# Optimization experiments

Hardware: AMD Instinct MI355X
Metric: run time of the kernel (lower is better)

The kernel has to match this reference:

```python
import jax, jax.numpy as jnp
import numpy as np

M = 16          # num_particles
EPS = 0.006


def setup_inputs() -> dict:
    key = jax.random.key(0)
    k1, k2, k3, k4 = jax.random.split(key, 4)
    B, P, O = 131072, 16, 4  # batch, pred_horizon, obs_horizon
    return {
        "ys_t": jax.random.normal(k1, (B, P, O), dtype=jnp.float32),
        "ys_r_stop": jax.random.normal(k2, (B, P, O), dtype=jnp.float32),
        "w_scale": jax.random.uniform(k3, (B,), dtype=jnp.float32),
        "time_weights": jax.random.uniform(k4, (B,), dtype=jnp.float32),
    }


def _laplace(a, b, ws, D):
    # a,b: [G, M, D]; ws: [G, M] (scale indexed by j, the first particle index)
    d = jnp.linalg.norm(a[:, :, None, :] - b[:, None, :, :], axis=-1)  # [G, M, M]
    d = jnp.maximum(d, EPS)
    return jnp.exp(-ws[:, :, None] * d / D)


def reference(ys_t, ys_r_stop, w_scale, time_weights):
    B = ys_t.shape[0]
    G = B // M
    x = ys_t.reshape(G, M, -1)        # [G, M, D]
    y = ys_r_stop.reshape(G, M, -1)   # [G, M, D]
    D = x.shape[-1]                   # pred_horizon * obs_horizon (dim_normalize)
    ws = w_scale.reshape(G, M)
    tw = time_weights.reshape(G, M)[:, 0]  # [G]
    terms = _laplace(x, x, ws, D) + _laplace(y, y, ws, D) - 2.0 * _laplace(x, y, ws, D)
    group_loss = terms.sum(axis=(1, 2)) * tw / (M * M)  # [G]
    return group_loss.sum() / G
```

## Files before the change

### kernel.cpp

```cpp
#include <hip/hip_runtime.h>


#define EPS_D 0.006f

#define ROT(v, O) __int_as_float(__builtin_amdgcn_update_dpp(              \
        0, __float_as_int(v), 0x120 + (O), 0xF, 0xF, false))

__global__ __launch_bounds__(256, 4)
void imm_loss_kernel(const float* __restrict__ ys_t,
                     const float* __restrict__ ys_r,
                     const float* __restrict__ w_scale,
                     const float* __restrict__ time_w,
                     float* __restrict__ partials)
{
    const int tid  = threadIdx.x;
    const int lane = tid & 63;
    const int wave = tid >> 6;
    const int g    = blockIdx.x * 4 + wave;
    const int j    = lane & 15;
    const int db   = lane >> 4;

    __shared__ float4 lds4[4][512];

    const float4* xg = reinterpret_cast<const float4*>(ys_t + (size_t)g * 1024);
    const float4* yg = reinterpret_cast<const float4*>(ys_r + (size_t)g * 1024);

    float4 xs[4], yv[4];
    #pragma unroll
    for (int k = 0; k < 4; ++k) {
        const int r  = 4 * k + db;
        const int gq = j ^ (r & 7);
        xs[k] = xg[r * 16 + gq];
        yv[k] = yg[r * 16 + gq];
    }
    #pragma unroll
    for (int k = 0; k < 4; ++k) {
        lds4[wave][k * 64 + lane]       = xs[k];
        lds4[wave][256 + k * 64 + lane] = yv[k];
    }

    const float s_j = w_scale[g * 16 + j] * (1.0f / 64.0f);
    const float tw  = time_w[g * 16];

    float xarr[16], yarr[16];
    #pragma unroll
    for (int m = 0; m < 4; ++m) {
        const int sl = (db * 4 + m) ^ (j & 7);
        const float4 xv = lds4[wave][j * 16 + sl];
        const float4 yw = lds4[wave][256 + j * 16 + sl];
        xarr[4*m+0] = xv.x; xarr[4*m+1] = xv.y; xarr[4*m+2] = xv.z; xarr[4*m+3] = xv.w;
        yarr[4*m+0] = yw.x; yarr[4*m+1] = yw.y; yarr[4*m+2] = yw.z; yarr[4*m+3] = yw.w;
    }

    float nx = 0.f, ny = 0.f, g0 = 0.f;
    float gxx[8], gyy[8], gxy[8], hxy[7];
    #pragma unroll
    for (int i = 0; i < 8; ++i) { gxx[i] = 0.f; gyy[i] = 0.f; gxy[i] = 0.f; }
    #pragma unroll
    for (int i = 0; i < 7; ++i) hxy[i] = 0.f;

#define ACC_FULL(O) {                                                      \
            const float xr = ROT(xd, O);                                   \
            const float yr = ROT(yd, O);                                   \
            gxx[(O)-1] = fmaf(xr, xd, gxx[(O)-1]);                         \
            gyy[(O)-1] = fmaf(yr, yd, gyy[(O)-1]);                         \
            gxy[(O)-1] = fmaf(yr, xd, gxy[(O)-1]); }
#define ACC_XY(O) {                                                        \
            const float yr = ROT(yd, O);                                   \
            hxy[(O)-9] = fmaf(yr, xd, hxy[(O)-9]); }

    #pragma unroll
    for (int d = 0; d < 16; ++d) {
        const float xd = xarr[d], yd = yarr[d];
        nx = fmaf(xd, xd, nx);
        ny = fmaf(yd, yd, ny);
        g0 = fmaf(xd, yd, g0);
        ACC_FULL(1) ACC_FULL(2) ACC_FULL(3) ACC_FULL(4)
        ACC_FULL(5) ACC_FULL(6) ACC_FULL(7) ACC_FULL(8)
        ACC_XY(9)  ACC_XY(10) ACC_XY(11) ACC_XY(12)
        ACC_XY(13) ACC_XY(14) ACC_XY(15)
    }

#define RED(v) { v += __shfl_xor(v, 16, 64); v += __shfl_xor(v, 32, 64); }
    RED(nx) RED(ny) RED(g0)
    #pragma unroll
    for (int i = 0; i < 8; ++i) { RED(gxx[i]) RED(gyy[i]) RED(gxy[i]) }
    #pragma unroll
    for (int i = 0; i < 7; ++i) { RED(hxy[i]) }

    float acc = 2.0f * __expf(-s_j * EPS_D);

    {
        const float d2 = fmaxf(nx + ny - 2.0f * g0, 0.0f);
        const float dd = fmaxf(sqrtf(d2), EPS_D);
        acc -= 2.0f * __expf(-s_j * dd);
    }

#define FIN_FULL(O, W) {                                                   \
        const float sk  = ROT(s_j, O);                                     \
        const float nxr = ROT(nx, O);                                      \
        const float nyr = ROT(ny, O);                                      \
        const float ddx = fmaxf(sqrtf(fmaxf(nx + nxr - 2.0f*gxx[(O)-1], 0.f)), EPS_D); \
        const float ddy = fmaxf(sqrtf(fmaxf(ny + nyr - 2.0f*gyy[(O)-1], 0.f)), EPS_D); \
        const float ddz = fmaxf(sqrtf(fmaxf(nx + nyr - 2.0f*gxy[(O)-1], 0.f)), EPS_D); \
        acc += (W) * (__expf(-s_j * ddx) + __expf(-sk * ddx));             \
        acc += (W) * (__expf(-s_j * ddy) + __expf(-sk * ddy));             \
        acc -= 2.0f * __expf(-s_j * ddz); }

#define FIN_XY(O) {                                                        \
        const float nyr = ROT(ny, O);                                      \
        const float ddz = fmaxf(sqrtf(fmaxf(nx + nyr - 2.0f*hxy[(O)-9], 0.f)), EPS_D); \
        acc -= 2.0f * __expf(-s_j * ddz); }

    FIN_FULL(1, 1.0f)
    FIN_FULL(2, 1.0f)
    FIN_FULL(3, 1.0f)
    FIN_FULL(4, 1.0f)
    FIN_FULL(5, 1.0f)
    FIN_FULL(6, 1.0f)
    FIN_FULL(7, 1.0f)
    FIN_FULL(8, 0.5f)
    FIN_XY(9)
    FIN_XY(10)
    FIN_XY(11)
    FIN_XY(12)
    FIN_XY(13)
    FIN_XY(14)
    FIN_XY(15)

    float val = acc * tw;
    #pragma unroll
    for (int off = 32; off; off >>= 1)
        val += __shfl_xor(val, off, 64);

    __shared__ float smem[4];
    if (lane == 0) smem[wave] = val;
    __syncthreads();
    if (tid == 0)
        partials[blockIdx.x] = smem[0] + smem[1] + smem[2] + smem[3];
}

__global__ void imm_reduce_kernel(const float* __restrict__ part, int n,
                                  float inv_scale, float* __restrict__ out)
{
    const int tid = threadIdx.x;
    float v = 0.f;
    for (int i = tid; i < n; i += 256) v += part[i];
    #pragma unroll
    for (int off = 32; off; off >>= 1) v += __shfl_xor(v, off, 64);
    __shared__ float s[4];
    if ((tid & 63) == 0) s[tid >> 6] = v;
    __syncthreads();
    if (tid == 0) out[0] = (s[0] + s[1] + s[2] + s[3]) * inv_scale;
}

extern "C" void kernel_launch(void* const* d_in, const int* in_sizes, int n_in,
                              void* d_out, int out_size, void* d_ws, size_t ws_size,
                              hipStream_t stream)
{
    const float* ys_t = (const float*)d_in[0];
    const float* ys_r = (const float*)d_in[1];
    const float* wsc  = (const float*)d_in[2];
    const float* twp  = (const float*)d_in[3];
    float* out      = (float*)d_out;
    float* partials = (float*)d_ws;

    const int B = in_sizes[2];
    const int G = B / 16;
    const int blocks = G / 4;

    imm_loss_kernel<<<blocks, 256, 0, stream>>>(ys_t, ys_r, wsc, twp, partials);

    const float inv_scale = 1.0f / (1024.0f * (float)G);
    imm_reduce_kernel<<<1, 256, 0, stream>>>(partials, blocks, inv_scale, out);
}
```

Measured before the change: 122.3 us.

## Halve LDS staging, stream y from LDS, use exp2 and swizzle reductions

Shrinks the per-wave LDS staging buffer by reusing it: x is transposed first, then the buffer is overwritten with y, which is read back in chunks inside the Gram accumulation instead of being held in a full 16-register array. Launch bounds are raised to 8 blocks per CU to allow higher occupancy with the reduced LDS and register footprint. Exponentials become raw exp2 with log2(e) folded into the scale, and xor-16 and lower cross-lane reductions use ds_swizzle instead of generic shuffles. The risks are register spills under the tighter launch bound, and that overwriting the buffer with y while other lanes may still be reading x relies on the wave executing in lockstep, since there is no barrier between them.

```diff
diff --git a/kernel.cpp b/kernel.cpp
--- a/kernel.cpp
+++ b/kernel.cpp
@@ -2,11 +2,21 @@
 
 
 #define EPS_D 0.006f
+#define L2E_D64 0.022542110013890053f
+#define EXP2(x) __builtin_amdgcn_exp2f(x)
 
 #define ROT(v, O) __int_as_float(__builtin_amdgcn_update_dpp(              \
         0, __float_as_int(v), 0x120 + (O), 0xF, 0xF, false))
 
-__global__ __launch_bounds__(256, 4)
+#define SWZ(v, PAT) __int_as_float(__builtin_amdgcn_ds_swizzle(            \
+        __float_as_int(v), PAT))
+#define XOR16(v) SWZ(v, 0x401F)
+#define XOR8(v)  SWZ(v, 0x201F)
+#define XOR4(v)  SWZ(v, 0x101F)
+#define XOR2(v)  SWZ(v, 0x081F)
+#define XOR1(v)  SWZ(v, 0x041F)
+
+__global__ __launch_bounds__(256, 8)
 void imm_loss_kernel(const float* __restrict__ ys_t,
                      const float* __restrict__ ys_r,
                      const float* __restrict__ w_scale,
@@ -20,7 +30,8 @@
     const int j    = lane & 15;
     const int db   = lane >> 4;
 
-    __shared__ float4 lds4[4][512];
+    __shared__ float4 lds4[4][256];
+    __shared__ float smem[4];
 
     const float4* xg = reinterpret_cast<const float4*>(ys_t + (size_t)g * 1024);
     const float4* yg = reinterpret_cast<const float4*>(ys_r + (size_t)g * 1024);
@@ -33,24 +44,23 @@
         xs[k] = xg[r * 16 + gq];
         yv[k] = yg[r * 16 + gq];
     }
-    #pragma unroll
-    for (int k = 0; k < 4; ++k) {
-        lds4[wave][k * 64 + lane]       = xs[k];
-        lds4[wave][256 + k * 64 + lane] = yv[k];
-    }
 
-    const float s_j = w_scale[g * 16 + j] * (1.0f / 64.0f);
+    const float s_j = w_scale[g * 16 + j] * L2E_D64;
     const float tw  = time_w[g * 16];
 
-    float xarr[16], yarr[16];
+    #pragma unroll
+    for (int k = 0; k < 4; ++k) lds4[wave][k * 64 + lane] = xs[k];
+
+    float xarr[16];
     #pragma unroll
     for (int m = 0; m < 4; ++m) {
         const int sl = (db * 4 + m) ^ (j & 7);
-        const float4 xv = lds4[wave][j * 16 + sl];
-        const float4 yw = lds4[wave][256 + j * 16 + sl];
-        xarr[4*m+0] = xv.x; xarr[4*m+1] = xv.y; xarr[4*m+2] = xv.z; xarr[4*m+3] = xv.w;
-        yarr[4*m+0] = yw.x; yarr[4*m+1] = yw.y; yarr[4*m+2] = yw.z; yarr[4*m+3] = yw.w;
+        const float4 v = lds4[wave][j * 16 + sl];
+        xarr[4*m+0] = v.x; xarr[4*m+1] = v.y; xarr[4*m+2] = v.z; xarr[4*m+3] = v.w;
     }
+
+    #pragma unroll
+    for (int k = 0; k < 4; ++k) lds4[wave][k * 64 + lane] = yv[k];
 
     float nx = 0.f, ny = 0.f, g0 = 0.f;
     float gxx[8], gyy[8], gxy[8], hxy[7];
@@ -69,31 +79,41 @@
             const float yr = ROT(yd, O);                                   \
             hxy[(O)-9] = fmaf(yr, xd, hxy[(O)-9]); }
 
-    #pragma unroll
-    for (int d = 0; d < 16; ++d) {
-        const float xd = xarr[d], yd = yarr[d];
-        nx = fmaf(xd, xd, nx);
-        ny = fmaf(yd, yd, ny);
-        g0 = fmaf(xd, yd, g0);
-        ACC_FULL(1) ACC_FULL(2) ACC_FULL(3) ACC_FULL(4)
-        ACC_FULL(5) ACC_FULL(6) ACC_FULL(7) ACC_FULL(8)
-        ACC_XY(9)  ACC_XY(10) ACC_XY(11) ACC_XY(12)
-        ACC_XY(13) ACC_XY(14) ACC_XY(15)
-    }
+#define GRAM4(M) {                                                         \
+        const int sl = (db * 4 + (M)) ^ (j & 7);                           \
+        const float4 wv = lds4[wave][j * 16 + sl];                         \
+        _Pragma("unroll")                                                  \
+        for (int e = 0; e < 4; ++e) {                                      \
+            const float xd = xarr[4*(M)+e];                                \
+            const float yd = (e == 0) ? wv.x : (e == 1) ? wv.y             \
+                           : (e == 2) ? wv.z : wv.w;                       \
+            nx = fmaf(xd, xd, nx);                                         \
+            ny = fmaf(yd, yd, ny);                                         \
+            g0 = fmaf(xd, yd, g0);                                         \
+            ACC_FULL(1) ACC_FULL(2) ACC_FULL(3) ACC_FULL(4)                \
+            ACC_FULL(5) ACC_FULL(6) ACC_FULL(7) ACC_FULL(8)                \
+            ACC_XY(9)  ACC_XY(10) ACC_XY(11) ACC_XY(12)                    \
+            ACC_XY(13) ACC_XY(14) ACC_XY(15)                               \
+        } }
 
-#define RED(v) { v += __shfl_xor(v, 16, 64); v += __shfl_xor(v, 32, 64); }
+    GRAM4(0)
+    GRAM4(1)
+    GRAM4(2)
+    GRAM4(3)
+
+#define RED(v) { v += XOR16(v); v += __shfl_xor(v, 32, 64); }
     RED(nx) RED(ny) RED(g0)
     #pragma unroll
     for (int i = 0; i < 8; ++i) { RED(gxx[i]) RED(gyy[i]) RED(gxy[i]) }
     #pragma unroll
     for (int i = 0; i < 7; ++i) { RED(hxy[i]) }
 
-    float acc = 2.0f * __expf(-s_j * EPS_D);
+    float acc = 2.0f * EXP2(-s_j * EPS_D);
 
     {
         const float d2 = fmaxf(nx + ny - 2.0f * g0, 0.0f);
         const float dd = fmaxf(sqrtf(d2), EPS_D);
-        acc -= 2.0f * __expf(-s_j * dd);
+        acc -= 2.0f * EXP2(-s_j * dd);
     }
 
 #define FIN_FULL(O, W) {                                                   \
@@ -103,14 +123,14 @@
         const float ddx = fmaxf(sqrtf(fmaxf(nx + nxr - 2.0f*gxx[(O)-1], 0.f)), EPS_D); \
         const float ddy = fmaxf(sqrtf(fmaxf(ny + nyr - 2.0f*gyy[(O)-1], 0.f)), EPS_D); \
         const float ddz = fmaxf(sqrtf(fmaxf(nx + nyr - 2.0f*gxy[(O)-1], 0.f)), EPS_D); \
-        acc += (W) * (__expf(-s_j * ddx) + __expf(-sk * ddx));             \
-        acc += (W) * (__expf(-s_j * ddy) + __expf(-sk * ddy));             \
-        acc -= 2.0f * __expf(-s_j * ddz); }
+        acc += (W) * (EXP2(-s_j * ddx) + EXP2(-sk * ddx));                 \
+        acc += (W) * (EXP2(-s_j * ddy) + EXP2(-sk * ddy));                 \
+        acc -= 2.0f * EXP2(-s_j * ddz); }
 
 #define FIN_XY(O) {                                                        \
         const float nyr = ROT(ny, O);                                      \
         const float ddz = fmaxf(sqrtf(fmaxf(nx + nyr - 2.0f*hxy[(O)-9], 0.f)), EPS_D); \
-        acc -= 2.0f * __expf(-s_j * ddz); }
+        acc -= 2.0f * EXP2(-s_j * ddz); }
 
     FIN_FULL(1, 1.0f)
     FIN_FULL(2, 1.0f)
@@ -129,11 +149,13 @@
     FIN_XY(15)
 
     float val = acc * tw;
-    #pragma unroll
-    for (int off = 32; off; off >>= 1)
-        val += __shfl_xor(val, off, 64);
+    val += __shfl_xor(val, 32, 64);
+    val += XOR16(val);
+    val += XOR8(val);
+    val += XOR4(val);
+    val += XOR2(val);
+    val += XOR1(val);
 
-    __shared__ float smem[4];
     if (lane == 0) smem[wave] = val;
     __syncthreads();
     if (tid == 0)
```

Result: slower. 139.4 us (+14.0%).
